# Performance work log

Hardware: AMD Instinct MI355X
Metric: run time of the kernel (lower is better)

The kernel has to match this reference:

```python
import jax, jax.numpy as jnp
import numpy as np

C, H, W, N = 3, 512, 512, 64


def setup_inputs() -> dict:
    key = jax.random.key(0)
    k1, k2 = jax.random.split(key)
    img = jax.random.uniform(k1, (C, H, W), dtype=jnp.float32)
    theta = jax.random.uniform(k2, (N,), dtype=jnp.float32) * 2.0 * np.pi
    return {"img": img, "theta": theta}


def reference(img, theta):
    # img: (C, H, W); theta: (N,) angles in radians ('rotate' branch).
    Ci, Hi, Wi = img.shape
    n = theta.shape[0]
    cos_t = jnp.cos(theta)[:, None, None]  # (N,1,1)
    sin_t = jnp.sin(theta)[:, None, None]
    # affine_grid with align_corners=True: base coords linspace(-1,1) over W (x) and H (y)
    xs = jnp.linspace(-1.0, 1.0, Wi, dtype=img.dtype)
    ys = jnp.linspace(-1.0, 1.0, Hi, dtype=img.dtype)
    x, y = jnp.meshgrid(xs, ys)  # (H, W), xy indexing
    # inv_rotation = [[cos, -sin, 0], [sin, cos, 0]]
    gx = cos_t * x - sin_t * y  # (N, H, W) normalized sample x
    gy = sin_t * x + cos_t * y  # (N, H, W) normalized sample y
    # grid_sample bilinear, padding_mode='zeros', align_corners=True
    ix = (gx + 1.0) * 0.5 * (Wi - 1)
    iy = (gy + 1.0) * 0.5 * (Hi - 1)
    x0 = jnp.floor(ix)
    y0 = jnp.floor(iy)
    x1 = x0 + 1.0
    y1 = y0 + 1.0
    wx = ix - x0  # frac weights
    wy = iy - y0

    def gather(yc, xc):
        valid = (xc >= 0) & (xc <= Wi - 1) & (yc >= 0) & (yc <= Hi - 1)
        xi = jnp.clip(xc, 0, Wi - 1).astype(jnp.int32)
        yi = jnp.clip(yc, 0, Hi - 1).astype(jnp.int32)
        v = img[:, yi, xi]  # (C, N, H, W)
        return v * valid[None].astype(img.dtype)

    out = (gather(y0, x0) * ((1.0 - wx) * (1.0 - wy))[None]
           + gather(y0, x1) * (wx * (1.0 - wy))[None]
           + gather(y1, x0) * ((1.0 - wx) * wy)[None]
           + gather(y1, x1) * (wx * wy)[None])  # (C, N, H, W)
    return jnp.transpose(out, (1, 0, 2, 3))  # (N, C, H, W)
```

## Files before the change

### kernel.cpp

```cpp
#include <hip/hip_runtime.h>

typedef float f4 __attribute__((ext_vector_type(4)));

constexpr int Hh = 512;
constexpr int Ww = 512;
constexpr int Nn = 64;
constexpr int HW = Hh * Ww;
constexpr int TS   = 32;
constexpr int ROWS = 48;
constexpr int COLS = 52;

__global__ void precompute_cs(const float* __restrict__ theta,
                              float* __restrict__ cs) {
    int t = threadIdx.x;
    if (t < Nn) {
        float th = theta[t];
        cs[2 * t]     = cosf(th);
        cs[2 * t + 1] = sinf(th);
    }
}

__device__ __forceinline__ int swz(int lr, int lc) {
    return lr * COLS + (lc ^ (lr & 3));
}

__global__ __launch_bounds__(256) void rot_bilinear_lds(
        const float* __restrict__ img,
        const float* __restrict__ cs,
        float* __restrict__ out)
{
    __shared__ f4 lds[ROWS * COLS];

    const int n   = blockIdx.y;
    const int tix = blockIdx.x & 15;
    const int tiy = blockIdx.x >> 4;
    const int i0  = tiy * TS;
    const int j0  = tix * TS;

    const float c = cs[2 * n];
    const float s = cs[2 * n + 1];
    const float A = 255.5f * (1.0f - c + s);
    const float B = 255.5f * (1.0f - s - c);

    const float j0f = (float)j0, j1f = (float)(j0 + TS - 1);
    const float i0f = (float)i0, i1f = (float)(i0 + TS - 1);
    const float x00 = fmaf(c, j0f, fmaf(-s, i0f, A));
    const float x01 = fmaf(c, j1f, fmaf(-s, i0f, A));
    const float x10 = fmaf(c, j0f, fmaf(-s, i1f, A));
    const float x11 = fmaf(c, j1f, fmaf(-s, i1f, A));
    const float y00 = fmaf(s, j0f, fmaf(c, i0f, B));
    const float y01 = fmaf(s, j1f, fmaf(c, i0f, B));
    const float y10 = fmaf(s, j0f, fmaf(c, i1f, B));
    const float y11 = fmaf(s, j1f, fmaf(c, i1f, B));
    const float minx = fminf(fminf(x00, x01), fminf(x10, x11));
    const float maxx = fmaxf(fmaxf(x00, x01), fmaxf(x10, x11));
    const float miny = fminf(fminf(y00, y01), fminf(y10, y11));
    const float maxy = fmaxf(fmaxf(y00, y01), fmaxf(y10, y11));

    const int cmin = (int)floorf(minx) - 1;
    const int cmax = (int)floorf(maxx) + 2;
    const int rmin = (int)floorf(miny) - 1;
    const int rmax = (int)floorf(maxy) + 2;
    const int c0s = min(max(cmin, 0), 511);
    const int c1s = min(max(cmax, 0), 511);
    const int r0s = min(max(rmin, 0), 511);
    const int r1s = min(max(rmax, 0), 511);
    const int c0a = c0s & ~3;
    const int width = c1s - c0a + 1;
    const int R     = r1s - r0s + 1;
    const bool interior = (cmin >= 0) & (rmin >= 0) & (cmax <= 511) & (rmax <= 511);

    const int tid = threadIdx.x;
    const int ty = tid >> 4, tx = tid & 15;
    const int cA = tx << 2;
    if (cA < width) {
        for (int rr = ty; rr < R; rr += 16) {
            const float* p = img + (r0s + rr) * Ww + c0a + cA;
            const f4 a0 = *(const f4*)p;
            const f4 a1 = *(const f4*)(p + HW);
            const f4 a2 = *(const f4*)(p + 2 * HW);
            #pragma unroll
            for (int e = 0; e < 4; ++e) {
                f4 v;
                v.x = a0[e]; v.y = a1[e]; v.z = a2[e]; v.w = 0.0f;
                lds[swz(rr, cA + e)] = v;
            }
        }
    }
    __syncthreads();

    const int ir  = tid >> 3;
    const int gj0 = j0 + ((tid & 7) << 2);
    const int gi  = i0 + ir;
    const float fi  = (float)gi;
    const float ixr = fmaf(-s, fi, A);
    const float iyr = fmaf( c, fi, B);

    f4 res[4];

    if (interior) {
        #pragma unroll
        for (int e = 0; e < 4; ++e) {
            const float fj = (float)(gj0 + e);
            const float ix = fmaf(c, fj, ixr);
            const float iy = fmaf(s, fj, iyr);
            const float x0f = floorf(ix), y0f = floorf(iy);
            const float wx = ix - x0f,  wy = iy - y0f;
            const int xi = (int)x0f - c0a;
            const int yi = (int)y0f - r0s;
            const float u0 = 1.0f - wx, v0 = 1.0f - wy;
            const float w00 = u0 * v0, w01 = wx * v0, w10 = u0 * wy, w11 = wx * wy;
            const int m0 = yi & 3, m1 = (yi + 1) & 3;
            const int rb0 = yi * COLS, rb1 = rb0 + COLS;
            const f4 v00 = lds[rb0 + ( xi      ^ m0)];
            const f4 v01 = lds[rb0 + ((xi + 1) ^ m0)];
            const f4 v10 = lds[rb1 + ( xi      ^ m1)];
            const f4 v11 = lds[rb1 + ((xi + 1) ^ m1)];
            res[e] = v00 * w00 + v01 * w01 + v10 * w10 + v11 * w11;
        }
    } else {
        #pragma unroll
        for (int e = 0; e < 4; ++e) {
            const float fj = (float)(gj0 + e);
            const float ix = fmaf(c, fj, ixr);
            const float iy = fmaf(s, fj, iyr);
            const float x0f = floorf(ix), y0f = floorf(iy);
            const float wx = ix - x0f,  wy = iy - y0f;
            const float x1f = x0f + 1.0f, y1f = y0f + 1.0f;

            const bool vx0 = (x0f >= 0.0f) && (x0f <= 511.0f);
            const bool vx1 = (x1f >= 0.0f) && (x1f <= 511.0f);
            const bool vy0 = (y0f >= 0.0f) && (y0f <= 511.0f);
            const bool vy1 = (y1f >= 0.0f) && (y1f <= 511.0f);

            const int xi0 = min(max((int)x0f,     0), 511) - c0a;
            const int xi1 = min(max((int)x0f + 1, 0), 511) - c0a;
            const int yi0 = min(max((int)y0f,     0), 511) - r0s;
            const int yi1 = min(max((int)y0f + 1, 0), 511) - r0s;

            float w00 = (1.0f - wx) * (1.0f - wy); if (!(vx0 && vy0)) w00 = 0.0f;
            float w01 = wx * (1.0f - wy);          if (!(vx1 && vy0)) w01 = 0.0f;
            float w10 = (1.0f - wx) * wy;          if (!(vx0 && vy1)) w10 = 0.0f;
            float w11 = wx * wy;                   if (!(vx1 && vy1)) w11 = 0.0f;

            const f4 v00 = lds[swz(yi0, xi0)];
            const f4 v01 = lds[swz(yi0, xi1)];
            const f4 v10 = lds[swz(yi1, xi0)];
            const f4 v11 = lds[swz(yi1, xi1)];
            res[e] = v00 * w00 + v01 * w01 + v10 * w10 + v11 * w11;
        }
    }

    const size_t base = (size_t)n * (size_t)(3 * HW) + (size_t)gi * Ww + gj0;
    *(float4*)&out[base]          = make_float4(res[0].x, res[1].x, res[2].x, res[3].x);
    *(float4*)&out[base + HW]     = make_float4(res[0].y, res[1].y, res[2].y, res[3].y);
    *(float4*)&out[base + 2 * HW] = make_float4(res[0].z, res[1].z, res[2].z, res[3].z);
}

extern "C" void kernel_launch(void* const* d_in, const int* in_sizes, int n_in,
                              void* d_out, int out_size, void* d_ws, size_t ws_size,
                              hipStream_t stream) {
    const float* img   = (const float*)d_in[0];
    const float* theta = (const float*)d_in[1];
    float*       out   = (float*)d_out;
    float*       cs    = (float*)d_ws;

    precompute_cs<<<1, 64, 0, stream>>>(theta, cs);

    dim3 grid((Hh / TS) * (Ww / TS), Nn);
    rot_bilinear_lds<<<grid, 256, 0, stream>>>(img, cs, out);
}
```

Baseline: 221.0 us.

## Shrink rotation tiles to 16x16 with one output pixel per thread

Cuts the output tile from 32x32 to 16x16 and shrinks the LDS staging buffer to match. Each thread now computes one pixel instead of four, the loader does a single pass, and the LDS swizzle changes from XOR-3 to XOR-7. A minimum-occupancy hint of 8 blocks per CU is added to the launch bounds. The goal is more blocks in flight and less LDS per block, but the halo-to-tile ratio grows, so more input is loaded per output pixel, and stores drop from float4 to scalar writes with shorter contiguous segments.

```diff
diff --git a/kernel.cpp b/kernel.cpp
--- a/kernel.cpp
+++ b/kernel.cpp
@@ -6,9 +6,9 @@
 constexpr int Ww = 512;
 constexpr int Nn = 64;
 constexpr int HW = Hh * Ww;
-constexpr int TS   = 32;
-constexpr int ROWS = 48;
-constexpr int COLS = 52;
+constexpr int TS   = 16;
+constexpr int ROWS = 26;
+constexpr int COLS = 32;
 
 __global__ void precompute_cs(const float* __restrict__ theta,
                               float* __restrict__ cs) {
@@ -21,10 +21,10 @@
 }
 
 __device__ __forceinline__ int swz(int lr, int lc) {
-    return lr * COLS + (lc ^ (lr & 3));
+    return lr * COLS + (lc ^ (lr & 7));
 }
 
-__global__ __launch_bounds__(256) void rot_bilinear_lds(
+__global__ __launch_bounds__(256, 8) void rot_bilinear_lds16(
         const float* __restrict__ img,
         const float* __restrict__ cs,
         float* __restrict__ out)
@@ -32,8 +32,8 @@
     __shared__ f4 lds[ROWS * COLS];
 
     const int n   = blockIdx.y;
-    const int tix = blockIdx.x & 15;
-    const int tiy = blockIdx.x >> 4;
+    const int tix = blockIdx.x & 31;
+    const int tiy = blockIdx.x >> 5;
     const int i0  = tiy * TS;
     const int j0  = tix * TS;
 
@@ -71,90 +71,78 @@
     const bool interior = (cmin >= 0) & (rmin >= 0) & (cmax <= 511) & (rmax <= 511);
 
     const int tid = threadIdx.x;
-    const int ty = tid >> 4, tx = tid & 15;
-    const int cA = tx << 2;
-    if (cA < width) {
-        for (int rr = ty; rr < R; rr += 16) {
-            const float* p = img + (r0s + rr) * Ww + c0a + cA;
-            const f4 a0 = *(const f4*)p;
-            const f4 a1 = *(const f4*)(p + HW);
-            const f4 a2 = *(const f4*)(p + 2 * HW);
-            #pragma unroll
-            for (int e = 0; e < 4; ++e) {
-                f4 v;
-                v.x = a0[e]; v.y = a1[e]; v.z = a2[e]; v.w = 0.0f;
-                lds[swz(rr, cA + e)] = v;
-            }
+    const int ty = tid >> 3;
+    const int cA = (tid & 7) << 2;
+    if (ty < R && cA < width) {
+        const float* p = img + (r0s + ty) * Ww + c0a + cA;
+        const f4 a0 = *(const f4*)p;
+        const f4 a1 = *(const f4*)(p + HW);
+        const f4 a2 = *(const f4*)(p + 2 * HW);
+        #pragma unroll
+        for (int e = 0; e < 4; ++e) {
+            f4 v;
+            v.x = a0[e]; v.y = a1[e]; v.z = a2[e]; v.w = 0.0f;
+            lds[swz(ty, cA + e)] = v;
         }
     }
     __syncthreads();
 
-    const int ir  = tid >> 3;
-    const int gj0 = j0 + ((tid & 7) << 2);
-    const int gi  = i0 + ir;
-    const float fi  = (float)gi;
-    const float ixr = fmaf(-s, fi, A);
-    const float iyr = fmaf( c, fi, B);
+    const int row = tid >> 4;
+    const int col = tid & 15;
+    const int gi  = i0 + row;
+    const int gj  = j0 + col;
+    const float fi = (float)gi, fj = (float)gj;
 
-    f4 res[4];
+    const float ix = fmaf(c, fj, fmaf(-s, fi, A));
+    const float iy = fmaf(s, fj, fmaf(c, fi, B));
+
+    f4 res;
 
     if (interior) {
-        #pragma unroll
-        for (int e = 0; e < 4; ++e) {
-            const float fj = (float)(gj0 + e);
-            const float ix = fmaf(c, fj, ixr);
-            const float iy = fmaf(s, fj, iyr);
-            const float x0f = floorf(ix), y0f = floorf(iy);
-            const float wx = ix - x0f,  wy = iy - y0f;
-            const int xi = (int)x0f - c0a;
-            const int yi = (int)y0f - r0s;
-            const float u0 = 1.0f - wx, v0 = 1.0f - wy;
-            const float w00 = u0 * v0, w01 = wx * v0, w10 = u0 * wy, w11 = wx * wy;
-            const int m0 = yi & 3, m1 = (yi + 1) & 3;
-            const int rb0 = yi * COLS, rb1 = rb0 + COLS;
-            const f4 v00 = lds[rb0 + ( xi      ^ m0)];
-            const f4 v01 = lds[rb0 + ((xi + 1) ^ m0)];
-            const f4 v10 = lds[rb1 + ( xi      ^ m1)];
-            const f4 v11 = lds[rb1 + ((xi + 1) ^ m1)];
-            res[e] = v00 * w00 + v01 * w01 + v10 * w10 + v11 * w11;
-        }
+        const float x0f = floorf(ix), y0f = floorf(iy);
+        const float wx = ix - x0f,  wy = iy - y0f;
+        const int xi = (int)x0f - c0a;
+        const int yi = (int)y0f - r0s;
+        const float u0 = 1.0f - wx, v0 = 1.0f - wy;
+        const float w00 = u0 * v0, w01 = wx * v0, w10 = u0 * wy, w11 = wx * wy;
+        const int m0 = yi & 7, m1 = (yi + 1) & 7;
+        const int rb0 = yi * COLS, rb1 = rb0 + COLS;
+        const f4 v00 = lds[rb0 + ( xi      ^ m0)];
+        const f4 v01 = lds[rb0 + ((xi + 1) ^ m0)];
+        const f4 v10 = lds[rb1 + ( xi      ^ m1)];
+        const f4 v11 = lds[rb1 + ((xi + 1) ^ m1)];
+        res = v00 * w00 + v01 * w01 + v10 * w10 + v11 * w11;
     } else {
-        #pragma unroll
-        for (int e = 0; e < 4; ++e) {
-            const float fj = (float)(gj0 + e);
-            const float ix = fmaf(c, fj, ixr);
-            const float iy = fmaf(s, fj, iyr);
-            const float x0f = floorf(ix), y0f = floorf(iy);
-            const float wx = ix - x0f,  wy = iy - y0f;
-            const float x1f = x0f + 1.0f, y1f = y0f + 1.0f;
+        const float x0f = floorf(ix), y0f = floorf(iy);
+        const float wx = ix - x0f,  wy = iy - y0f;
+        const float x1f = x0f + 1.0f, y1f = y0f + 1.0f;
 
-            const bool vx0 = (x0f >= 0.0f) && (x0f <= 511.0f);
-            const bool vx1 = (x1f >= 0.0f) && (x1f <= 511.0f);
-            const bool vy0 = (y0f >= 0.0f) && (y0f <= 511.0f);
-            const bool vy1 = (y1f >= 0.0f) && (y1f <= 511.0f);
+        const bool vx0 = (x0f >= 0.0f) && (x0f <= 511.0f);
+        const bool vx1 = (x1f >= 0.0f) && (x1f <= 511.0f);
+        const bool vy0 = (y0f >= 0.0f) && (y0f <= 511.0f);
+        const bool vy1 = (y1f >= 0.0f) && (y1f <= 511.0f);
 
-            const int xi0 = min(max((int)x0f,     0), 511) - c0a;
-            const int xi1 = min(max((int)x0f + 1, 0), 511) - c0a;
-            const int yi0 = min(max((int)y0f,     0), 511) - r0s;
-            const int yi1 = min(max((int)y0f + 1, 0), 511) - r0s;
+        const int xi0 = min(max((int)x0f,     0), 511) - c0a;
+        const int xi1 = min(max((int)x0f + 1, 0), 511) - c0a;
+        const int yi0 = min(max((int)y0f,     0), 511) - r0s;
+        const int yi1 = min(max((int)y0f + 1, 0), 511) - r0s;
 
-            float w00 = (1.0f - wx) * (1.0f - wy); if (!(vx0 && vy0)) w00 = 0.0f;
-            float w01 = wx * (1.0f - wy);          if (!(vx1 && vy0)) w01 = 0.0f;
-            float w10 = (1.0f - wx) * wy;          if (!(vx0 && vy1)) w10 = 0.0f;
-            float w11 = wx * wy;                   if (!(vx1 && vy1)) w11 = 0.0f;
+        float w00 = (1.0f - wx) * (1.0f - wy); if (!(vx0 && vy0)) w00 = 0.0f;
+        float w01 = wx * (1.0f - wy);          if (!(vx1 && vy0)) w01 = 0.0f;
+        float w10 = (1.0f - wx) * wy;          if (!(vx0 && vy1)) w10 = 0.0f;
+        float w11 = wx * wy;                   if (!(vx1 && vy1)) w11 = 0.0f;
 
-            const f4 v00 = lds[swz(yi0, xi0)];
-            const f4 v01 = lds[swz(yi0, xi1)];
-            const f4 v10 = lds[swz(yi1, xi0)];
-            const f4 v11 = lds[swz(yi1, xi1)];
-            res[e] = v00 * w00 + v01 * w01 + v10 * w10 + v11 * w11;
-        }
+        const f4 v00 = lds[swz(yi0, xi0)];
+        const f4 v01 = lds[swz(yi0, xi1)];
+        const f4 v10 = lds[swz(yi1, xi0)];
+        const f4 v11 = lds[swz(yi1, xi1)];
+        res = v00 * w00 + v01 * w01 + v10 * w10 + v11 * w11;
     }
 
-    const size_t base = (size_t)n * (size_t)(3 * HW) + (size_t)gi * Ww + gj0;
-    *(float4*)&out[base]          = make_float4(res[0].x, res[1].x, res[2].x, res[3].x);
-    *(float4*)&out[base + HW]     = make_float4(res[0].y, res[1].y, res[2].y, res[3].y);
-    *(float4*)&out[base + 2 * HW] = make_float4(res[0].z, res[1].z, res[2].z, res[3].z);
+    const size_t base = (size_t)n * (size_t)(3 * HW) + (size_t)gi * Ww + gj;
+    out[base]          = res.x;
+    out[base + HW]     = res.y;
+    out[base + 2 * HW] = res.z;
 }
 
 extern "C" void kernel_launch(void* const* d_in, const int* in_sizes, int n_in,
@@ -168,5 +156,5 @@
     precompute_cs<<<1, 64, 0, stream>>>(theta, cs);
 
     dim3 grid((Hh / TS) * (Ww / TS), Nn);
-    rot_bilinear_lds<<<grid, 256, 0, stream>>>(img, cs, out);
+    rot_bilinear_lds16<<<grid, 256, 0, stream>>>(img, cs, out);
 }
```

New measurement: 227.9 us. 1.03x slower.
